# Kernel optimization log

Hardware: AMD Instinct MI355X
Metric: run time of the kernel (lower is better)

## Reference

```python
import jax, jax.numpy as jnp
import numpy as np
import math

WS = 11
SIGMA = 1.5

def _gaussian_window(ws=WS, sigma=SIGMA):
    i = np.arange(ws)
    g = np.exp(-((i - ws // 2) ** 2) / (2.0 * sigma ** 2))
    g = (g / g.sum()).astype(np.float32)
    w2d = np.outer(g, g)  # [ws, ws]
    return jnp.asarray(w2d)

def _depthwise_conv(x, win2d):
    # x: [B, C, H, W]; win2d: [ws, ws]
    C = x.shape[1]
    kernel = jnp.broadcast_to(win2d[None, None], (C, 1, WS, WS)).astype(x.dtype)  # [C,1,ws,ws]
    return jax.lax.conv_general_dilated(
        x, kernel,
        window_strides=(1, 1),
        padding=[(WS // 2, WS // 2), (WS // 2, WS // 2)],
        dimension_numbers=("NCHW", "OIHW", "NCHW"),
        feature_group_count=C,
    )

def setup_inputs() -> dict:
    key = jax.random.key(0)
    k1, k2, k3 = jax.random.split(key, 3)
    B, C, H, W = 16, 3, 512, 512
    x = jax.random.uniform(k1, (B, C, H, W), dtype=jnp.float32)
    y = jax.random.uniform(k2, (B, C, H, W), dtype=jnp.float32)
    conf = jax.random.uniform(k3, (B, 1, H, W), dtype=jnp.float32)
    return {"x": x, "y": y, "conf": conf}

def reference(x, y, conf):
    win2d = _gaussian_window()
    mu_x = _depthwise_conv(x, win2d)
    mu_y = _depthwise_conv(y, win2d)
    mu_x2, mu_y2, mu_xy = mu_x * mu_x, mu_y * mu_y, mu_x * mu_y
    sigma_x2 = _depthwise_conv(x * x, win2d) - mu_x2
    sigma_y2 = _depthwise_conv(y * y, win2d) - mu_y2
    sigma_xy = _depthwise_conv(x * y, win2d) - mu_xy
    C1, C2 = 0.01 ** 2, 0.03 ** 2
    ssim = (2 * mu_xy + C1) * (2 * sigma_xy + C2) / ((mu_x2 + mu_y2 + C1) * (sigma_x2 + sigma_y2 + C2))
    loss_map = jnp.clip(1.0 - ssim, 0.0, 1.0)
    loss_map = loss_map * conf  # broadcast over channels
    return jnp.mean(loss_map)
```

## Files before the change

kernel.cpp:

```cpp
#include <hip/hip_runtime.h>
#include <cmath>

#define TW 32
#define TH 32
#define HR (TH + 10)
#define IMG 512
#define SSIM_C1 1e-4f
#define SSIM_C2 9e-4f

struct GaussWin { float g[11]; };

typedef float v2f __attribute__((ext_vector_type(2)));

__device__ __forceinline__ v2f pk_fma(v2f a, v2f b, v2f c) {
    return __builtin_elementwise_fma(a, b, c);
}
__device__ __forceinline__ v2f pk_mul(v2f a, v2f b) { return a * b; }

__launch_bounds__(256, 6)
__global__ void ssim_tile_kernel(const float* __restrict__ x,
                                 const float* __restrict__ y,
                                 const float* __restrict__ conf,
                                 float* __restrict__ partials,
                                 float* __restrict__ out,
                                 int use_ws, float scale,
                                 GaussWin W) {
    __shared__ float4 s_h4[HR * TW];
    __shared__ float  s_h1[HR * TW];
    __shared__ float  s_red[4];

    const int tid = threadIdx.x;
    const int plane = blockIdx.z;
    const int tx0 = blockIdx.x * TW;
    const int ty0 = blockIdx.y * TH;
    const int pbase = plane * (IMG * IMG);
    const int cbase = (plane / 3) * (IMG * IMG);

    constexpr int WI[11] = {0,1,2,3,4,5,4,3,2,1,0};
    v2f w2[6];
    #pragma unroll
    for (int i = 0; i < 6; i++) w2[i] = (v2f){W.g[i], W.g[i]};

    const bool interior = (blockIdx.x >= 1) & (blockIdx.x <= 14) &
                          (blockIdx.y >= 1) & (blockIdx.y <= 14);

    if (tid < HR * 4) {
        const int r = tid >> 2;
        const int cs = (tid & 3) * 8;
        const int gy = ty0 - 5 + r;
        const float* xrow = x + pbase + gy * IMG;
        const float* yrow = y + pbase + gy * IMG;
        const int c0 = tx0 + cs - 8;

        float4 fx[6], fy[6];
        if (interior) {
            #pragma unroll
            for (int q = 0; q < 6; q++) {
                fx[q] = *(const float4*)(xrow + c0 + 4 * q);
                fy[q] = *(const float4*)(yrow + c0 + 4 * q);
            }
        } else {
            const bool rowok = ((unsigned)gy < IMG);
            #pragma unroll
            for (int q = 0; q < 6; q++) {
                int col = c0 + 4 * q;
                fx[q] = make_float4(0.f, 0.f, 0.f, 0.f);
                fy[q] = make_float4(0.f, 0.f, 0.f, 0.f);
                if (rowok && (unsigned)col <= (unsigned)(IMG - 4)) {
                    fx[q] = *(const float4*)(xrow + col);
                    fy[q] = *(const float4*)(yrow + col);
                }
            }
        }
        float vxa[24], vya[24];
        #pragma unroll
        for (int q = 0; q < 6; q++) {
            vxa[4*q+0]=fx[q].x; vxa[4*q+1]=fx[q].y; vxa[4*q+2]=fx[q].z; vxa[4*q+3]=fx[q].w;
            vya[4*q+0]=fy[q].x; vya[4*q+1]=fy[q].y; vya[4*q+2]=fy[q].z; vya[4*q+3]=fy[q].w;
        }

        v2f amu[8], as2[8];
        float axy[8];
        #pragma unroll
        for (int j = 0; j < 8; j++) { amu[j]=(v2f){0.f,0.f}; as2[j]=(v2f){0.f,0.f}; axy[j]=0.f; }
        #pragma unroll
        for (int k = 0; k < 18; k++) {
            float xv = vxa[k + 3], yv = vya[k + 3];
            v2f xy = (v2f){xv, yv};
            v2f p2 = pk_mul(xy, xy);
            float pxy = xv * yv;
            const int jlo = (k - 10 > 0) ? (k - 10) : 0;
            const int jhi = (k < 7) ? k : 7;
            #pragma unroll
            for (int j = jlo; j <= jhi; j++) {
                v2f w = w2[WI[k - j]];
                amu[j] = pk_fma(xy, w, amu[j]);
                as2[j] = pk_fma(p2, w, as2[j]);
                axy[j] = fmaf(pxy, w.x, axy[j]);
            }
        }
        const int quad = cs & 24;
        const int base0 = cs + 2 * (cs >> 3) + 5 * r;
        #pragma unroll
        for (int j = 0; j < 8; j++) {
            int pc = quad | ((base0 + j) & 7);
            s_h4[r * TW + pc] = make_float4(amu[j].x, amu[j].y, as2[j].x, as2[j].y);
            s_h1[r * TW + pc] = axy[j];
        }
    }

    const int c  = tid & 31;
    const int r0 = (tid >> 5) * 4;
    float cf[4];
    #pragma unroll
    for (int j = 0; j < 4; j++) {
        cf[j] = conf[cbase + (ty0 + r0 + j) * IMG + tx0 + c];
    }
    __syncthreads();

    float ge[12];
    #pragma unroll
    for (int i = 0; i < 11; i++) ge[i] = W.g[WI[i]];
    ge[11] = 0.f;
    v2f wp[12];
    #pragma unroll
    for (int d = 0; d < 12; d++) wp[d] = (v2f){ ge[d], (d == 0) ? 0.f : ge[d - 1] };

    v2f amu[4], as2[4], axy2[2];
    #pragma unroll
    for (int j = 0; j < 4; j++) { amu[j]=(v2f){0.f,0.f}; as2[j]=(v2f){0.f,0.f}; }
    axy2[0] = (v2f){0.f, 0.f};
    axy2[1] = (v2f){0.f, 0.f};

    const int cquad = c & 24;
    const int cb0 = c + 2 * (c >> 3) + 5 * r0;
    #pragma unroll
    for (int t = 0; t < 14; t++) {
        int row = r0 + t;
        int pc = cquad | ((cb0 + 5 * t) & 7);
        float4 h4 = s_h4[row * TW + pc];
        float  h1 = s_h1[row * TW + pc];
        v2f hmu = (v2f){h4.x, h4.y};
        v2f hs2 = (v2f){h4.z, h4.w};
        #pragma unroll
        for (int j = 0; j < 4; j++) {
            int k = t - j;
            if (k >= 0 && k <= 10) {
                v2f w = w2[WI[k]];
                amu[j] = pk_fma(hmu, w, amu[j]);
                as2[j] = pk_fma(hs2, w, as2[j]);
            }
        }
        v2f h1b = (v2f){h1, h1};
        #pragma unroll
        for (int p = 0; p < 2; p++) {
            int d = t - 2 * p;
            if (d >= 0 && d <= 11) {
                axy2[p] = pk_fma(h1b, wp[d], axy2[p]);
            }
        }
    }

    float lsum = 0.f;
    #pragma unroll
    for (int j = 0; j < 4; j++) {
        float mu_x = amu[j].x, mu_y = amu[j].y;
        float axyj = (j & 1) ? axy2[j >> 1].y : axy2[j >> 1].x;
        v2f prod = pk_mul(amu[j], amu[j]);
        float mu_xy = mu_x * mu_y;
        v2f sig = as2[j] - prod;
        float sigxy = axyj - mu_xy;
        float num = fmaf(2.f, mu_xy, SSIM_C1) * fmaf(2.f, sigxy, SSIM_C2);
        float den = (prod.x + prod.y + SSIM_C1) * (sig.x + sig.y + SSIM_C2);
        float ssim = num * __builtin_amdgcn_rcpf(den);
        float loss = fminf(fmaxf(1.f - ssim, 0.f), 1.f);
        lsum = fmaf(loss, cf[j], lsum);
    }

    #pragma unroll
    for (int off = 32; off; off >>= 1) lsum += __shfl_down(lsum, off, 64);
    if ((tid & 63) == 0) s_red[tid >> 6] = lsum;
    __syncthreads();
    if (tid == 0) {
        float t = s_red[0] + s_red[1] + s_red[2] + s_red[3];
        if (use_ws) {
            partials[blockIdx.x + gridDim.x * (blockIdx.y + gridDim.y * blockIdx.z)] = t;
        } else {
            atomicAdd(out, t * scale);
        }
    }
}

__global__ void reduce_kernel(const float* __restrict__ partials, int n,
                              float* __restrict__ out, float scale) {
    __shared__ float s_red[16];
    float s = 0.f;
    const float4* p4 = (const float4*)partials;
    const int n4 = n >> 2;
    for (int i = threadIdx.x; i < n4; i += 1024) {
        float4 v = p4[i];
        s += (v.x + v.y) + (v.z + v.w);
    }
    for (int i = (n4 << 2) + threadIdx.x; i < n; i += 1024) s += partials[i];
    #pragma unroll
    for (int off = 32; off; off >>= 1) s += __shfl_down(s, off, 64);
    if ((threadIdx.x & 63) == 0) s_red[threadIdx.x >> 6] = s;
    __syncthreads();
    if (threadIdx.x == 0) {
        float t = 0.f;
        #pragma unroll
        for (int i = 0; i < 16; i++) t += s_red[i];
        out[0] = t * scale;
    }
}

extern "C" void kernel_launch(void* const* d_in, const int* in_sizes, int n_in,
                              void* d_out, int out_size, void* d_ws, size_t ws_size,
                              hipStream_t stream) {
    const float* x    = (const float*)d_in[0];
    const float* y    = (const float*)d_in[1];
    const float* conf = (const float*)d_in[2];
    float* out = (float*)d_out;
    float* partials = (float*)d_ws;

    GaussWin W;
    {
        double gd[11], s = 0.0;
        for (int i = 0; i < 11; i++) { gd[i] = exp(-((i - 5) * (i - 5)) / 4.5); s += gd[i]; }
        for (int i = 0; i < 11; i++) W.g[i] = (float)(gd[i] / s);
    }

    const int B = 16, C = 3;
    const float scale = 1.0f / (float)(B * C * IMG * IMG);
    dim3 grid(IMG / TW, IMG / TH, B * C);
    const int nblocks = (IMG / TW) * (IMG / TH) * B * C;
    const int use_ws = (ws_size >= (size_t)nblocks * sizeof(float)) ? 1 : 0;

    if (!use_ws) {
        hipMemsetAsync(d_out, 0, sizeof(float), stream);
    }
    ssim_tile_kernel<<<grid, 256, 0, stream>>>(x, y, conf, partials, out, use_ws, scale, W);
    if (use_ws) {
        reduce_kernel<<<1, 1024, 0, stream>>>(partials, nblocks, out, scale);
    }
}
```

Before: 164.5 us.

## Convolve x²+y² sum instead of separate squares, pack with xy into one float4

Since SSIM only needs sigma_x2 + sigma_y2, the kernel now convolves x²+y² as a single channel and packs it with x·y into one v2f accumulator. This drops from five to four convolved channels, removes the separate scalar shared array and its extra LDS traffic, and removes the odd packed-weight vertical path for xy. Register pressure falls, so launch bounds are raised to 7 blocks per SM for more occupancy. The trade-off is a slightly different rounding order in the variance sum.

```diff
diff --git a/kernel.cpp b/kernel.cpp
--- a/kernel.cpp
+++ b/kernel.cpp
@@ -15,9 +15,8 @@
 __device__ __forceinline__ v2f pk_fma(v2f a, v2f b, v2f c) {
     return __builtin_elementwise_fma(a, b, c);
 }
-__device__ __forceinline__ v2f pk_mul(v2f a, v2f b) { return a * b; }
-
-__launch_bounds__(256, 6)
+
+__launch_bounds__(256, 7)
 __global__ void ssim_tile_kernel(const float* __restrict__ x,
                                  const float* __restrict__ y,
                                  const float* __restrict__ conf,
@@ -25,8 +24,7 @@
                                  float* __restrict__ out,
                                  int use_ws, float scale,
                                  GaussWin W) {
-    __shared__ float4 s_h4[HR * TW];
-    __shared__ float  s_h1[HR * TW];
+    __shared__ float4 s_h[HR * TW];
     __shared__ float  s_red[4];
 
     const int tid = threadIdx.x;
@@ -79,24 +77,22 @@
             vya[4*q+0]=fy[q].x; vya[4*q+1]=fy[q].y; vya[4*q+2]=fy[q].z; vya[4*q+3]=fy[q].w;
         }
 
-        v2f amu[8], as2[8];
-        float axy[8];
-        #pragma unroll
-        for (int j = 0; j < 8; j++) { amu[j]=(v2f){0.f,0.f}; as2[j]=(v2f){0.f,0.f}; axy[j]=0.f; }
+        v2f amu[8], a2[8];
+        #pragma unroll
+        for (int j = 0; j < 8; j++) { amu[j]=(v2f){0.f,0.f}; a2[j]=(v2f){0.f,0.f}; }
         #pragma unroll
         for (int k = 0; k < 18; k++) {
             float xv = vxa[k + 3], yv = vya[k + 3];
             v2f xy = (v2f){xv, yv};
-            v2f p2 = pk_mul(xy, xy);
-            float pxy = xv * yv;
+            v2f p2 = xy * xy;
+            v2f zw = (v2f){p2.x + p2.y, xv * yv};
             const int jlo = (k - 10 > 0) ? (k - 10) : 0;
             const int jhi = (k < 7) ? k : 7;
             #pragma unroll
             for (int j = jlo; j <= jhi; j++) {
                 v2f w = w2[WI[k - j]];
                 amu[j] = pk_fma(xy, w, amu[j]);
-                as2[j] = pk_fma(p2, w, as2[j]);
-                axy[j] = fmaf(pxy, w.x, axy[j]);
+                a2[j]  = pk_fma(zw, w, a2[j]);
             }
         }
         const int quad = cs & 24;
@@ -104,8 +100,7 @@
         #pragma unroll
         for (int j = 0; j < 8; j++) {
             int pc = quad | ((base0 + j) & 7);
-            s_h4[r * TW + pc] = make_float4(amu[j].x, amu[j].y, as2[j].x, as2[j].y);
-            s_h1[r * TW + pc] = axy[j];
+            s_h[r * TW + pc] = make_float4(amu[j].x, amu[j].y, a2[j].x, a2[j].y);
         }
     }
 
@@ -118,19 +113,9 @@
     }
     __syncthreads();
 
-    float ge[12];
-    #pragma unroll
-    for (int i = 0; i < 11; i++) ge[i] = W.g[WI[i]];
-    ge[11] = 0.f;
-    v2f wp[12];
-    #pragma unroll
-    for (int d = 0; d < 12; d++) wp[d] = (v2f){ ge[d], (d == 0) ? 0.f : ge[d - 1] };
-
-    v2f amu[4], as2[4], axy2[2];
-    #pragma unroll
-    for (int j = 0; j < 4; j++) { amu[j]=(v2f){0.f,0.f}; as2[j]=(v2f){0.f,0.f}; }
-    axy2[0] = (v2f){0.f, 0.f};
-    axy2[1] = (v2f){0.f, 0.f};
+    v2f amu[4], a2[4];
+    #pragma unroll
+    for (int j = 0; j < 4; j++) { amu[j]=(v2f){0.f,0.f}; a2[j]=(v2f){0.f,0.f}; }
 
     const int cquad = c & 24;
     const int cb0 = c + 2 * (c >> 3) + 5 * r0;
@@ -138,25 +123,16 @@
     for (int t = 0; t < 14; t++) {
         int row = r0 + t;
         int pc = cquad | ((cb0 + 5 * t) & 7);
-        float4 h4 = s_h4[row * TW + pc];
-        float  h1 = s_h1[row * TW + pc];
+        float4 h4 = s_h[row * TW + pc];
         v2f hmu = (v2f){h4.x, h4.y};
-        v2f hs2 = (v2f){h4.z, h4.w};
+        v2f h2  = (v2f){h4.z, h4.w};
         #pragma unroll
         for (int j = 0; j < 4; j++) {
             int k = t - j;
             if (k >= 0 && k <= 10) {
                 v2f w = w2[WI[k]];
                 amu[j] = pk_fma(hmu, w, amu[j]);
-                as2[j] = pk_fma(hs2, w, as2[j]);
-            }
-        }
-        v2f h1b = (v2f){h1, h1};
-        #pragma unroll
-        for (int p = 0; p < 2; p++) {
-            int d = t - 2 * p;
-            if (d >= 0 && d <= 11) {
-                axy2[p] = pk_fma(h1b, wp[d], axy2[p]);
+                a2[j]  = pk_fma(h2, w, a2[j]);
             }
         }
     }
@@ -165,13 +141,13 @@
     #pragma unroll
     for (int j = 0; j < 4; j++) {
         float mu_x = amu[j].x, mu_y = amu[j].y;
-        float axyj = (j & 1) ? axy2[j >> 1].y : axy2[j >> 1].x;
-        v2f prod = pk_mul(amu[j], amu[j]);
+        v2f prod = amu[j] * amu[j];
         float mu_xy = mu_x * mu_y;
-        v2f sig = as2[j] - prod;
-        float sigxy = axyj - mu_xy;
+        float musq  = prod.x + prod.y;
+        float sigsum = a2[j].x - musq;
+        float sigxy  = a2[j].y - mu_xy;
         float num = fmaf(2.f, mu_xy, SSIM_C1) * fmaf(2.f, sigxy, SSIM_C2);
-        float den = (prod.x + prod.y + SSIM_C1) * (sig.x + sig.y + SSIM_C2);
+        float den = (musq + SSIM_C1) * (sigsum + SSIM_C2);
         float ssim = num * __builtin_amdgcn_rcpf(den);
         float loss = fminf(fmaxf(1.f - ssim, 0.f), 1.f);
         lsum = fmaf(loss, cf[j], lsum);
```

New measurement: 156.0 us. 5.1% less time.
